# Kernel optimization log

Measured on AMD Instinct MI355X. Metric: run time of the kernel, lower is better.

The kernel has to match this reference:

```python
import jax, jax.numpy as jnp
import numpy as np

D_MODEL = 1024
NUM_HEADS = 16
HEAD_DIM = D_MODEL // NUM_HEADS


def setup_inputs() -> dict:
    key = jax.random.key(0)
    kq, kk, kv, kw, kb = jax.random.split(key, 5)
    N, S = 2, 2048
    query = jax.random.normal(kq, (N, S, D_MODEL), dtype=jnp.float32)
    key_t = jax.random.normal(kk, (N, S, D_MODEL), dtype=jnp.float32)
    value = jax.random.normal(kv, (N, S, D_MODEL), dtype=jnp.float32)
    # fc_out params (nn.Linear(d_model, d_model)): W [out,in], b [out]
    lim = 1.0 / np.sqrt(D_MODEL)
    W_out = jax.random.uniform(kw, (D_MODEL, D_MODEL), minval=-lim, maxval=lim, dtype=jnp.float32)
    b_out = jax.random.uniform(kb, (D_MODEL,), minval=-lim, maxval=lim, dtype=jnp.float32)
    return {"query": query, "key": key_t, "value": value, "W_out": W_out, "b_out": b_out}


def reference(query, key, value, W_out, b_out):
    N, Lq, _ = query.shape
    Lk = key.shape[1]
    q = query.reshape(N, Lq, NUM_HEADS, HEAD_DIM)
    k = key.reshape(N, Lk, NUM_HEADS, HEAD_DIM)
    v = value.reshape(N, Lk, NUM_HEADS, HEAD_DIM)
    # NOTE: original module does NOT apply q/k/v Linear layers and does NOT scale by 1/sqrt(d)
    scores = jnp.einsum("nqhd,nkhd->nhqk", q, k)
    attn = jax.nn.softmax(scores, axis=3)
    out = jnp.einsum("nhqk,nkhd->nqhd", attn, v).reshape(N, Lq, D_MODEL)
    return out @ W_out.T + b_out
```

## Files before the change

### kernel.cpp

```cpp
#include <hip/hip_runtime.h>

typedef _Float16 half8 __attribute__((ext_vector_type(8)));
typedef _Float16 half4 __attribute__((ext_vector_type(4)));
typedef float f32x4 __attribute__((ext_vector_type(4)));

#define N_B 2
#define S_LEN 2048
#define NH 16
#define HD 64
#define DM 1024
#define LOG2E 1.44269504088896f

__device__ __forceinline__ void gload16(const void* g, void* l) {
    __builtin_amdgcn_global_load_lds(
        (const __attribute__((address_space(1))) unsigned int*)g,
        (__attribute__((address_space(3))) unsigned int*)l, 16, 0, 0);
}

__device__ __forceinline__ float fexp2(float x) {
    float r;
    asm("v_exp_f32 %0, %1" : "=v"(r) : "v"(x));
    return r;
}

__global__ __launch_bounds__(256) void k_prep(const float* __restrict__ K,
                                              const float* __restrict__ V,
                                              const float* __restrict__ Wo,
                                              _Float16* __restrict__ Kh,
                                              _Float16* __restrict__ Vt,
                                              _Float16* __restrict__ Wh) {
    __shared__ _Float16 tile[64][65];
    const int id = blockIdx.x;
    if (id < 4096) {
        int i = id * 256 + threadIdx.x;
        float4 v = ((const float4*)K)[i];
        int base = i * 4;
        int d = base & 63;
        int h = (base >> 6) & 15;
        int s = (base >> 10) & 2047;
        int n = base >> 21;
        size_t o = ((size_t)((n * NH + h) * S_LEN + s)) * HD + d;
        half4 hv = {(_Float16)v.x, (_Float16)v.y, (_Float16)v.z, (_Float16)v.w};
        *(half4*)(Kh + o) = hv;
    } else if (id < 5120) {
        int b = id - 4096;
        int st = b & 31, h = (b >> 5) & 15, n = b >> 9;
        int c = threadIdx.x & 63, r0 = threadIdx.x >> 6;
#pragma unroll
        for (int i = 0; i < 16; ++i) {
            int r = i * 4 + r0;
            tile[r][c] = (_Float16)V[((size_t)(n * S_LEN) + st * 64 + r) * DM + h * HD + c];
        }
        __syncthreads();
#pragma unroll
        for (int i = 0; i < 16; ++i) {
            int d = i * 4 + r0;
            Vt[((size_t)((n * NH + h) * HD + d)) * S_LEN + st * 64 + c] = tile[c][d];
        }
    } else {
        int i = (id - 5120) * 256 + threadIdx.x;
        float4 v = ((const float4*)Wo)[i];
        half4 hv = {(_Float16)v.x, (_Float16)v.y, (_Float16)v.z, (_Float16)v.w};
        *(half4*)(Wh + (size_t)i * 4) = hv;
    }
}

__global__ __launch_bounds__(256) void k_attn(const float* __restrict__ Q,
                                              const _Float16* __restrict__ Kh,
                                              const _Float16* __restrict__ Vth,
                                              _Float16* __restrict__ Oatt) {
    __shared__ _Float16 KT[2][64 * 64];
    __shared__ _Float16 VS[2][64 * 64];
    __shared__ _Float16 PL[4][16 * 64];

    const int id = blockIdx.x;
    const int xcd = id & 7;
    const int sl = id >> 3;
    const int nh = xcd + 8 * (sl >> 5);
    const int qt = sl & 31;

    const int tid = threadIdx.x;
    const int w = tid >> 6;
    const int lane = tid & 63;
    const int lr = lane & 15;
    const int lg = lane >> 4;
    const int lg4 = lg * 4;
    const int n = nh >> 4, h = nh & 15;

    const size_t head = (size_t)nh * S_LEN * HD;
    const char* Khead = (const char*)(Kh + head);
    const char* Vhead = (const char*)(Vth + head);

    const float* qrow = Q + ((size_t)(n * S_LEN) + qt * 64 + w * 16 + lr) * DM + h * HD + lg * 8;
    float4 qa = *(const float4*)(qrow);
    float4 qb = *(const float4*)(qrow + 4);
    float4 qc = *(const float4*)(qrow + 32);
    float4 qd = *(const float4*)(qrow + 36);
    half8 qf0 = {(_Float16)(qa.x * LOG2E), (_Float16)(qa.y * LOG2E),
                 (_Float16)(qa.z * LOG2E), (_Float16)(qa.w * LOG2E),
                 (_Float16)(qb.x * LOG2E), (_Float16)(qb.y * LOG2E),
                 (_Float16)(qb.z * LOG2E), (_Float16)(qb.w * LOG2E)};
    half8 qf1 = {(_Float16)(qc.x * LOG2E), (_Float16)(qc.y * LOG2E),
                 (_Float16)(qc.z * LOG2E), (_Float16)(qc.w * LOG2E),
                 (_Float16)(qd.x * LOG2E), (_Float16)(qd.y * LOG2E),
                 (_Float16)(qd.z * LOG2E), (_Float16)(qd.w * LOG2E)};

    f32x4 zero = {0.f, 0.f, 0.f, 0.f};
    f32x4 oacc[4] = {zero, zero, zero, zero};
    float m_q = -1e30f, l_q = 0.f;

    char* pl = (char*)&PL[w][0];
    const int pmask = (lr & 7) << 4;
    int pw0 = lr * 128 + ((0 * 32 + lg * 8) ^ pmask);
    int pw1 = lr * 128 + ((1 * 32 + lg * 8) ^ pmask);
    int pw2 = lr * 128 + ((2 * 32 + lg * 8) ^ pmask);
    int pw3 = lr * 128 + ((3 * 32 + lg * 8) ^ pmask);
    int pr0 = lr * 128 + ((lg * 16) ^ pmask);
    int pr1 = lr * 128 + ((64 + lg * 16) ^ pmask);

    const int rr = lane >> 3;
    const int cb = (lane & 7) * 16;
    const int gcb = cb ^ (rr << 4);

    auto STAGE = [&](int kt, int b) {
#pragma unroll
        for (int j = 0; j < 2; ++j) {
            int row = (w * 2 + j) * 8 + rr;
            gload16(Khead + ((size_t)(kt * 64 + row)) * 128 + gcb,
                    (char*)&KT[b][0] + (w * 2 + j) * 1024);
            gload16(Vhead + (size_t)row * 4096 + (size_t)kt * 128 + gcb,
                    (char*)&VS[b][0] + (w * 2 + j) * 1024);
        }
    };

    auto BODY = [&](int kt, int buf, bool do_stage) {
        if (do_stage) STAGE(kt + 1, buf ^ 1);

        const char* ldsK = (const char*)&KT[buf][0];
        const char* ldsV = (const char*)&VS[buf][0];

        f32x4 st[4] = {zero, zero, zero, zero};
#pragma unroll
        for (int nb = 0; nb < 4; ++nb) {
            int row = nb * 16 + lr;
            int sw = (row & 7) << 4;
            const char* kp = ldsK + row * 128;
            half8 kf0 = *(const half8*)(kp + ((lg * 16) ^ sw));
            half8 kf1 = *(const half8*)(kp + ((64 + lg * 16) ^ sw));
            st[nb] = __builtin_amdgcn_mfma_f32_16x16x32_f16(kf0, qf0, st[nb], 0, 0, 0);
            st[nb] = __builtin_amdgcn_mfma_f32_16x16x32_f16(kf1, qf1, st[nb], 0, 0, 0);
        }
        float t0 = fmaxf(fmaxf(st[0][0], st[0][1]), fmaxf(st[0][2], st[0][3]));
        float t1 = fmaxf(fmaxf(st[1][0], st[1][1]), fmaxf(st[1][2], st[1][3]));
        float t2 = fmaxf(fmaxf(st[2][0], st[2][1]), fmaxf(st[2][2], st[2][3]));
        float t3 = fmaxf(fmaxf(st[3][0], st[3][1]), fmaxf(st[3][2], st[3][3]));
        float tm = fmaxf(fmaxf(t0, t1), fmaxf(t2, t3));
        tm = fmaxf(tm, __shfl_xor(tm, 16));
        tm = fmaxf(tm, __shfl_xor(tm, 32));
        if (!__all(tm <= m_q + 8.f)) {
            float mn = fmaxf(m_q, tm);
            float sc = fexp2(m_q - mn);
            m_q = mn;
            l_q *= sc;
            float s0 = __shfl(sc, lg4 + 0);
            float s1 = __shfl(sc, lg4 + 1);
            float s2 = __shfl(sc, lg4 + 2);
            float s3 = __shfl(sc, lg4 + 3);
#pragma unroll
            for (int ob = 0; ob < 4; ++ob) {
                oacc[ob][0] *= s0; oacc[ob][1] *= s1;
                oacc[ob][2] *= s2; oacc[ob][3] *= s3;
            }
        }
        float rs = 0.f;
#pragma unroll
        for (int nb = 0; nb < 4; ++nb)
#pragma unroll
            for (int r = 0; r < 4; ++r) {
                float p = fexp2(st[nb][r] - m_q);
                st[nb][r] = p;
                rs += p;
            }
        rs += __shfl_xor(rs, 16);
        rs += __shfl_xor(rs, 32);
        l_q += rs;
        half4 p0 = {(_Float16)st[0][0], (_Float16)st[0][1], (_Float16)st[0][2], (_Float16)st[0][3]};
        half4 p1 = {(_Float16)st[1][0], (_Float16)st[1][1], (_Float16)st[1][2], (_Float16)st[1][3]};
        half4 p2 = {(_Float16)st[2][0], (_Float16)st[2][1], (_Float16)st[2][2], (_Float16)st[2][3]};
        half4 p3 = {(_Float16)st[3][0], (_Float16)st[3][1], (_Float16)st[3][2], (_Float16)st[3][3]};
        *(half4*)(pl + pw0) = p0;
        *(half4*)(pl + pw1) = p1;
        *(half4*)(pl + pw2) = p2;
        *(half4*)(pl + pw3) = p3;
        half8 pa0 = *(const half8*)(pl + pr0);
        half8 pa1 = *(const half8*)(pl + pr1);
#pragma unroll
        for (int ob = 0; ob < 4; ++ob) {
            int row = ob * 16 + lr;
            int sw = (row & 7) << 4;
            const char* vp = ldsV + row * 128;
            half8 vf0 = *(const half8*)(vp + ((lg * 16) ^ sw));
            half8 vf1 = *(const half8*)(vp + ((64 + lg * 16) ^ sw));
            oacc[ob] = __builtin_amdgcn_mfma_f32_16x16x32_f16(pa0, vf0, oacc[ob], 0, 0, 0);
            oacc[ob] = __builtin_amdgcn_mfma_f32_16x16x32_f16(pa1, vf1, oacc[ob], 0, 0, 0);
        }
        if (do_stage) __syncthreads();
    };

    STAGE(0, 0);
    __syncthreads();
    for (int t = 0; t < 31; ++t) BODY(t, t & 1, true);
    BODY(31, 1, false);

    float li0 = __shfl(l_q, lg4 + 0);
    float li1 = __shfl(l_q, lg4 + 1);
    float li2 = __shfl(l_q, lg4 + 2);
    float li3 = __shfl(l_q, lg4 + 3);
    float inv[4] = {1.f / li0, 1.f / li1, 1.f / li2, 1.f / li3};
#pragma unroll
    for (int i = 0; i < 4; ++i) {
        int q = qt * 64 + w * 16 + lg4 + i;
#pragma unroll
        for (int ob = 0; ob < 4; ++ob) {
            int d = ob * 16 + lr;
            Oatt[((size_t)(n * S_LEN + q)) * DM + h * HD + d] = (_Float16)(oacc[ob][i] * inv[i]);
        }
    }
}

__global__ __launch_bounds__(256) void k_proj(const _Float16* __restrict__ A,
                                              const _Float16* __restrict__ W,
                                              const float* __restrict__ bias,
                                              float* __restrict__ out) {
    __shared__ _Float16 As[2][128 * 64];
    __shared__ _Float16 Ws[2][128 * 64];

    const int id = blockIdx.x;
    const int ot = id & 7;
    const int mt = id >> 3;
    const int tid = threadIdx.x;
    const int w = tid >> 6;
    const int lane = tid & 63;
    const int lr = lane & 15, lg = lane >> 4;
    const int wm = (w >> 1) * 64, wn = (w & 1) * 64;

    const int rr = lane >> 3;
    const int cb = (lane & 7) * 16;
    const int gcb = cb ^ (rr << 4);

    const char* Abase = (const char*)(A + (size_t)(mt * 128) * DM);
    const char* Wbase = (const char*)(W + (size_t)(ot * 128) * DM);

    auto STAGE = [&](int kt, int b) {
#pragma unroll
        for (int r = 0; r < 4; ++r) {
            int row = r * 32 + w * 8 + rr;
            gload16(Abase + (size_t)row * 2048 + kt * 128 + gcb,
                    (char*)&As[b][0] + (r * 32 + w * 8) * 128);
            gload16(Wbase + (size_t)row * 2048 + kt * 128 + gcb,
                    (char*)&Ws[b][0] + (r * 32 + w * 8) * 128);
        }
    };

    f32x4 zero = {0.f, 0.f, 0.f, 0.f};
    f32x4 acc[4][4];
#pragma unroll
    for (int mi = 0; mi < 4; ++mi)
#pragma unroll
        for (int ni = 0; ni < 4; ++ni) acc[mi][ni] = zero;

    auto COMPUTE = [&](int b) {
        const char* ldsA = (const char*)&As[b][0];
        const char* ldsW = (const char*)&Ws[b][0];
        half8 af[4][2], wf[4][2];
#pragma unroll
        for (int mi = 0; mi < 4; ++mi) {
            int row = wm + mi * 16 + lr;
            int sw = (row & 7) << 4;
            const char* p = ldsA + row * 128;
            af[mi][0] = *(const half8*)(p + ((lg * 16) ^ sw));
            af[mi][1] = *(const half8*)(p + ((64 + lg * 16) ^ sw));
        }
#pragma unroll
        for (int ni = 0; ni < 4; ++ni) {
            int row = wn + ni * 16 + lr;
            int sw = (row & 7) << 4;
            const char* p = ldsW + row * 128;
            wf[ni][0] = *(const half8*)(p + ((lg * 16) ^ sw));
            wf[ni][1] = *(const half8*)(p + ((64 + lg * 16) ^ sw));
        }
#pragma unroll
        for (int mi = 0; mi < 4; ++mi)
#pragma unroll
            for (int ni = 0; ni < 4; ++ni) {
                acc[mi][ni] = __builtin_amdgcn_mfma_f32_16x16x32_f16(af[mi][0], wf[ni][0], acc[mi][ni], 0, 0, 0);
                acc[mi][ni] = __builtin_amdgcn_mfma_f32_16x16x32_f16(af[mi][1], wf[ni][1], acc[mi][ni], 0, 0, 0);
            }
    };

    STAGE(0, 0);
    __syncthreads();
    for (int kt = 0; kt < 15; ++kt) {
        STAGE(kt + 1, (kt & 1) ^ 1);
        COMPUTE(kt & 1);
        __syncthreads();
    }
    COMPUTE(1);

#pragma unroll
    for (int ni = 0; ni < 4; ++ni) {
        int o = ot * 128 + wn + ni * 16 + lr;
        float b = bias[o];
#pragma unroll
        for (int mi = 0; mi < 4; ++mi)
#pragma unroll
            for (int i = 0; i < 4; ++i) {
                int m = mt * 128 + wm + mi * 16 + lg * 4 + i;
                out[(size_t)m * DM + o] = acc[mi][ni][i] + b;
            }
    }
}

extern "C" void kernel_launch(void* const* d_in, const int* in_sizes, int n_in,
                              void* d_out, int out_size, void* d_ws, size_t ws_size,
                              hipStream_t stream) {
    const float* Q = (const float*)d_in[0];
    const float* K = (const float*)d_in[1];
    const float* V = (const float*)d_in[2];
    const float* Wo = (const float*)d_in[3];
    const float* bo = (const float*)d_in[4];
    float* out = (float*)d_out;
    char* ws = (char*)d_ws;

    _Float16* Kh = (_Float16*)(ws);
    _Float16* Vt = (_Float16*)(ws + (8u << 20));
    _Float16* Oatt = (_Float16*)(ws + (16u << 20));
    _Float16* Wh = (_Float16*)(ws + (24u << 20));

    k_prep<<<6144, 256, 0, stream>>>(K, V, Wo, Kh, Vt, Wh);
    k_attn<<<1024, 256, 0, stream>>>(Q, Kh, Vt, Oatt);
    k_proj<<<256, 256, 0, stream>>>(Oatt, Wh, bo, out);
}
```

Baseline: 101.3 us.

## Switch attention to 32x32x16 MFMA with 128-query tiles and register-only P

The attention kernel moves from 16x16x32 to 32x32x16 MFMA, so each wave now handles 32 queries and each block 128 queries, halving the grid to 512 blocks. Each K/V tile staged in LDS is therefore reused by twice as many queries. The probability matrix no longer round-trips through LDS; it is rearranged across lane halves with shuffles to form the A operand. The trade-offs are fewer blocks, which means less occupancy and parallelism across the device, higher register pressure from 16-wide accumulators, and ds_bpermute calls for per-row rescaling.

Measured after the change: 107.4 us. 1.06x slower.

```diff
diff --git a/kernel.cpp b/kernel.cpp
--- a/kernel.cpp
+++ b/kernel.cpp
@@ -3,6 +3,8 @@
 typedef _Float16 half8 __attribute__((ext_vector_type(8)));
 typedef _Float16 half4 __attribute__((ext_vector_type(4)));
 typedef float f32x4 __attribute__((ext_vector_type(4)));
+typedef float f32x16 __attribute__((ext_vector_type(16)));
+typedef unsigned u32x4 __attribute__((ext_vector_type(4)));
 
 #define N_B 2
 #define S_LEN 2048
@@ -71,52 +73,39 @@
                                               _Float16* __restrict__ Oatt) {
     __shared__ _Float16 KT[2][64 * 64];
     __shared__ _Float16 VS[2][64 * 64];
-    __shared__ _Float16 PL[4][16 * 64];
 
     const int id = blockIdx.x;
     const int xcd = id & 7;
     const int sl = id >> 3;
-    const int nh = xcd + 8 * (sl >> 5);
-    const int qt = sl & 31;
+    const int nh = xcd + 8 * (sl >> 4);
+    const int qt = sl & 15;
 
     const int tid = threadIdx.x;
     const int w = tid >> 6;
     const int lane = tid & 63;
-    const int lr = lane & 15;
-    const int lg = lane >> 4;
-    const int lg4 = lg * 4;
+    const int l31 = lane & 31;
+    const int hi = lane >> 5;
     const int n = nh >> 4, h = nh & 15;
 
     const size_t head = (size_t)nh * S_LEN * HD;
     const char* Khead = (const char*)(Kh + head);
     const char* Vhead = (const char*)(Vth + head);
 
-    const float* qrow = Q + ((size_t)(n * S_LEN) + qt * 64 + w * 16 + lr) * DM + h * HD + lg * 8;
-    float4 qa = *(const float4*)(qrow);
-    float4 qb = *(const float4*)(qrow + 4);
-    float4 qc = *(const float4*)(qrow + 32);
-    float4 qd = *(const float4*)(qrow + 36);
-    half8 qf0 = {(_Float16)(qa.x * LOG2E), (_Float16)(qa.y * LOG2E),
-                 (_Float16)(qa.z * LOG2E), (_Float16)(qa.w * LOG2E),
-                 (_Float16)(qb.x * LOG2E), (_Float16)(qb.y * LOG2E),
-                 (_Float16)(qb.z * LOG2E), (_Float16)(qb.w * LOG2E)};
-    half8 qf1 = {(_Float16)(qc.x * LOG2E), (_Float16)(qc.y * LOG2E),
-                 (_Float16)(qc.z * LOG2E), (_Float16)(qc.w * LOG2E),
-                 (_Float16)(qd.x * LOG2E), (_Float16)(qd.y * LOG2E),
-                 (_Float16)(qd.z * LOG2E), (_Float16)(qd.w * LOG2E)};
-
-    f32x4 zero = {0.f, 0.f, 0.f, 0.f};
-    f32x4 oacc[4] = {zero, zero, zero, zero};
+    const int qg = qt * 128 + w * 32 + l31;
+    const float* qbase = Q + ((size_t)(n * S_LEN) + qg) * DM + h * HD;
+    auto mkqf = [&](int c) -> half8 {
+        float4 a = *(const float4*)(qbase + 16 * c + 8 * hi);
+        float4 b = *(const float4*)(qbase + 16 * c + 8 * hi + 4);
+        half8 r = {(_Float16)(a.x * LOG2E), (_Float16)(a.y * LOG2E),
+                   (_Float16)(a.z * LOG2E), (_Float16)(a.w * LOG2E),
+                   (_Float16)(b.x * LOG2E), (_Float16)(b.y * LOG2E),
+                   (_Float16)(b.z * LOG2E), (_Float16)(b.w * LOG2E)};
+        return r;
+    };
+    half8 qf0 = mkqf(0), qf1 = mkqf(1), qf2 = mkqf(2), qf3 = mkqf(3);
+
+    f32x16 oacc0 = {}, oacc1 = {};
     float m_q = -1e30f, l_q = 0.f;
-
-    char* pl = (char*)&PL[w][0];
-    const int pmask = (lr & 7) << 4;
-    int pw0 = lr * 128 + ((0 * 32 + lg * 8) ^ pmask);
-    int pw1 = lr * 128 + ((1 * 32 + lg * 8) ^ pmask);
-    int pw2 = lr * 128 + ((2 * 32 + lg * 8) ^ pmask);
-    int pw3 = lr * 128 + ((3 * 32 + lg * 8) ^ pmask);
-    int pr0 = lr * 128 + ((lg * 16) ^ pmask);
-    int pr1 = lr * 128 + ((64 + lg * 16) ^ pmask);
 
     const int rr = lane >> 3;
     const int cb = (lane & 7) * 16;
@@ -133,77 +122,92 @@
         }
     };
 
+    const int rmask = (l31 & 7) << 4;
+    auto ldF = [&](const char* lds, int blk, int c) -> half8 {
+        int off = (32 * blk + l31) * 128 + ((32 * c + 16 * hi) ^ rmask);
+        return *(const half8*)(lds + off);
+    };
+
+    auto pk2 = [&](float a, float b) -> unsigned {
+        unsigned short ua = __builtin_bit_cast(unsigned short, (_Float16)a);
+        unsigned short ub = __builtin_bit_cast(unsigned short, (_Float16)b);
+        return (unsigned)ua | ((unsigned)ub << 16);
+    };
+    auto mkpa = [&](const f32x16& S, int rb) -> half8 {
+        unsigned w0 = pk2(S[rb + 0], S[rb + 1]);
+        unsigned w1 = pk2(S[rb + 2], S[rb + 3]);
+        unsigned w2 = pk2(S[rb + 4], S[rb + 5]);
+        unsigned w3 = pk2(S[rb + 6], S[rb + 7]);
+        unsigned x0 = (unsigned)__shfl_xor((int)w0, 32);
+        unsigned x1 = (unsigned)__shfl_xor((int)w1, 32);
+        unsigned x2 = (unsigned)__shfl_xor((int)w2, 32);
+        unsigned x3 = (unsigned)__shfl_xor((int)w3, 32);
+        u32x4 t;
+        t[0] = hi ? x2 : w0;
+        t[1] = hi ? x3 : w1;
+        t[2] = hi ? w2 : x0;
+        t[3] = hi ? w3 : x1;
+        return __builtin_bit_cast(half8, t);
+    };
+
     auto BODY = [&](int kt, int buf, bool do_stage) {
         if (do_stage) STAGE(kt + 1, buf ^ 1);
-
         const char* ldsK = (const char*)&KT[buf][0];
         const char* ldsV = (const char*)&VS[buf][0];
 
-        f32x4 st[4] = {zero, zero, zero, zero};
-#pragma unroll
-        for (int nb = 0; nb < 4; ++nb) {
-            int row = nb * 16 + lr;
-            int sw = (row & 7) << 4;
-            const char* kp = ldsK + row * 128;
-            half8 kf0 = *(const half8*)(kp + ((lg * 16) ^ sw));
-            half8 kf1 = *(const half8*)(kp + ((64 + lg * 16) ^ sw));
-            st[nb] = __builtin_amdgcn_mfma_f32_16x16x32_f16(kf0, qf0, st[nb], 0, 0, 0);
-            st[nb] = __builtin_amdgcn_mfma_f32_16x16x32_f16(kf1, qf1, st[nb], 0, 0, 0);
-        }
-        float t0 = fmaxf(fmaxf(st[0][0], st[0][1]), fmaxf(st[0][2], st[0][3]));
-        float t1 = fmaxf(fmaxf(st[1][0], st[1][1]), fmaxf(st[1][2], st[1][3]));
-        float t2 = fmaxf(fmaxf(st[2][0], st[2][1]), fmaxf(st[2][2], st[2][3]));
-        float t3 = fmaxf(fmaxf(st[3][0], st[3][1]), fmaxf(st[3][2], st[3][3]));
-        float tm = fmaxf(fmaxf(t0, t1), fmaxf(t2, t3));
-        tm = fmaxf(tm, __shfl_xor(tm, 16));
-        tm = fmaxf(tm, __shfl_xor(tm, 32));
+        f32x16 s0 = {}, s1 = {};
+        s0 = __builtin_amdgcn_mfma_f32_32x32x16_f16(ldF(ldsK, 0, 0), qf0, s0, 0, 0, 0);
+        s0 = __builtin_amdgcn_mfma_f32_32x32x16_f16(ldF(ldsK, 0, 1), qf1, s0, 0, 0, 0);
+        s0 = __builtin_amdgcn_mfma_f32_32x32x16_f16(ldF(ldsK, 0, 2), qf2, s0, 0, 0, 0);
+        s0 = __builtin_amdgcn_mfma_f32_32x32x16_f16(ldF(ldsK, 0, 3), qf3, s0, 0, 0, 0);
+        s1 = __builtin_amdgcn_mfma_f32_32x32x16_f16(ldF(ldsK, 1, 0), qf0, s1, 0, 0, 0);
+        s1 = __builtin_amdgcn_mfma_f32_32x32x16_f16(ldF(ldsK, 1, 1), qf1, s1, 0, 0, 0);
+        s1 = __builtin_amdgcn_mfma_f32_32x32x16_f16(ldF(ldsK, 1, 2), qf2, s1, 0, 0, 0);
+        s1 = __builtin_amdgcn_mfma_f32_32x32x16_f16(ldF(ldsK, 1, 3), qf3, s1, 0, 0, 0);
+
+        float mx[16];
+#pragma unroll
+        for (int i = 0; i < 16; ++i) mx[i] = fmaxf(s0[i], s1[i]);
+#pragma unroll
+        for (int st = 8; st > 0; st >>= 1)
+#pragma unroll
+            for (int i = 0; i < 8; ++i)
+                if (i < st) mx[i] = fmaxf(mx[i], mx[i + st]);
+        float tm = fmaxf(mx[0], __shfl_xor(mx[0], 32));
         if (!__all(tm <= m_q + 8.f)) {
             float mn = fmaxf(m_q, tm);
             float sc = fexp2(m_q - mn);
             m_q = mn;
             l_q *= sc;
-            float s0 = __shfl(sc, lg4 + 0);
-            float s1 = __shfl(sc, lg4 + 1);
-            float s2 = __shfl(sc, lg4 + 2);
-            float s3 = __shfl(sc, lg4 + 3);
-#pragma unroll
-            for (int ob = 0; ob < 4; ++ob) {
-                oacc[ob][0] *= s0; oacc[ob][1] *= s1;
-                oacc[ob][2] *= s2; oacc[ob][3] *= s3;
+            int scb = __builtin_bit_cast(int, sc);
+#pragma unroll
+            for (int r = 0; r < 16; ++r) {
+                int qr = (r & 3) + 8 * (r >> 2) + 4 * hi;
+                float s = __builtin_bit_cast(float, __builtin_amdgcn_ds_bpermute(4 * qr, scb));
+                oacc0[r] *= s;
+                oacc1[r] *= s;
             }
         }
         float rs = 0.f;
 #pragma unroll
-        for (int nb = 0; nb < 4; ++nb)
-#pragma unroll
-            for (int r = 0; r < 4; ++r) {
-                float p = fexp2(st[nb][r] - m_q);
-                st[nb][r] = p;
-                rs += p;
-            }
-        rs += __shfl_xor(rs, 16);
+        for (int i = 0; i < 16; ++i) { float p = fexp2(s0[i] - m_q); s0[i] = p; rs += p; }
+#pragma unroll
+        for (int i = 0; i < 16; ++i) { float p = fexp2(s1[i] - m_q); s1[i] = p; rs += p; }
         rs += __shfl_xor(rs, 32);
         l_q += rs;
-        half4 p0 = {(_Float16)st[0][0], (_Float16)st[0][1], (_Float16)st[0][2], (_Float16)st[0][3]};
-        half4 p1 = {(_Float16)st[1][0], (_Float16)st[1][1], (_Float16)st[1][2], (_Float16)st[1][3]};
-        half4 p2 = {(_Float16)st[2][0], (_Float16)st[2][1], (_Float16)st[2][2], (_Float16)st[2][3]};
-        half4 p3 = {(_Float16)st[3][0], (_Float16)st[3][1], (_Float16)st[3][2], (_Float16)st[3][3]};
-        *(half4*)(pl + pw0) = p0;
-        *(half4*)(pl + pw1) = p1;
-        *(half4*)(pl + pw2) = p2;
-        *(half4*)(pl + pw3) = p3;
-        half8 pa0 = *(const half8*)(pl + pr0);
-        half8 pa1 = *(const half8*)(pl + pr1);
-#pragma unroll
-        for (int ob = 0; ob < 4; ++ob) {
-            int row = ob * 16 + lr;
-            int sw = (row & 7) << 4;
-            const char* vp = ldsV + row * 128;
-            half8 vf0 = *(const half8*)(vp + ((lg * 16) ^ sw));
-            half8 vf1 = *(const half8*)(vp + ((64 + lg * 16) ^ sw));
-            oacc[ob] = __builtin_amdgcn_mfma_f32_16x16x32_f16(pa0, vf0, oacc[ob], 0, 0, 0);
-            oacc[ob] = __builtin_amdgcn_mfma_f32_16x16x32_f16(pa1, vf1, oacc[ob], 0, 0, 0);
-        }
+
+        half8 pa0 = mkpa(s0, 0), pa1 = mkpa(s0, 8);
+        half8 pa2 = mkpa(s1, 0), pa3 = mkpa(s1, 8);
+
+        oacc0 = __builtin_amdgcn_mfma_f32_32x32x16_f16(pa0, ldF(ldsV, 0, 0), oacc0, 0, 0, 0);
+        oacc0 = __builtin_amdgcn_mfma_f32_32x32x16_f16(pa1, ldF(ldsV, 0, 1), oacc0, 0, 0, 0);
+        oacc0 = __builtin_amdgcn_mfma_f32_32x32x16_f16(pa2, ldF(ldsV, 0, 2), oacc0, 0, 0, 0);
+        oacc0 = __builtin_amdgcn_mfma_f32_32x32x16_f16(pa3, ldF(ldsV, 0, 3), oacc0, 0, 0, 0);
+        oacc1 = __builtin_amdgcn_mfma_f32_32x32x16_f16(pa0, ldF(ldsV, 1, 0), oacc1, 0, 0, 0);
+        oacc1 = __builtin_amdgcn_mfma_f32_32x32x16_f16(pa1, ldF(ldsV, 1, 1), oacc1, 0, 0, 0);
+        oacc1 = __builtin_amdgcn_mfma_f32_32x32x16_f16(pa2, ldF(ldsV, 1, 2), oacc1, 0, 0, 0);
+        oacc1 = __builtin_amdgcn_mfma_f32_32x32x16_f16(pa3, ldF(ldsV, 1, 3), oacc1, 0, 0, 0);
+
         if (do_stage) __syncthreads();
     };
 
@@ -212,19 +216,16 @@
     for (int t = 0; t < 31; ++t) BODY(t, t & 1, true);
     BODY(31, 1, false);
 
-    float li0 = __shfl(l_q, lg4 + 0);
-    float li1 = __shfl(l_q, lg4 + 1);
-    float li2 = __shfl(l_q, lg4 + 2);
-    float li3 = __shfl(l_q, lg4 + 3);
-    float inv[4] = {1.f / li0, 1.f / li1, 1.f / li2, 1.f / li3};
-#pragma unroll
-    for (int i = 0; i < 4; ++i) {
-        int q = qt * 64 + w * 16 + lg4 + i;
-#pragma unroll
-        for (int ob = 0; ob < 4; ++ob) {
-            int d = ob * 16 + lr;
-            Oatt[((size_t)(n * S_LEN + q)) * DM + h * HD + d] = (_Float16)(oacc[ob][i] * inv[i]);
-        }
+    float rinv = 1.f / l_q;
+    int rb = __builtin_bit_cast(int, rinv);
+#pragma unroll
+    for (int r = 0; r < 16; ++r) {
+        int qr = (r & 3) + 8 * (r >> 2) + 4 * hi;
+        float iv = __builtin_bit_cast(float, __builtin_amdgcn_ds_bpermute(4 * qr, rb));
+        int qglob = qt * 128 + w * 32 + qr;
+        size_t base = ((size_t)(n * S_LEN + qglob)) * DM + h * HD + l31;
+        Oatt[base] = (_Float16)(oacc0[r] * iv);
+        Oatt[base + 32] = (_Float16)(oacc1[r] * iv);
     }
 }
 
@@ -338,6 +339,6 @@
     _Float16* Wh = (_Float16*)(ws + (24u << 20));
 
     k_prep<<<6144, 256, 0, stream>>>(K, V, Wo, Kh, Vt, Wh);
-    k_attn<<<1024, 256, 0, stream>>>(Q, Kh, Vt, Oatt);
+    k_attn<<<512, 256, 0, stream>>>(Q, Kh, Vt, Oatt);
     k_proj<<<256, 256, 0, stream>>>(Oatt, Wh, bo, out);
 }
```
